# Kernel optimization log

Hardware: AMD Instinct MI355X
Metric: run time of the kernel (lower is better)

Reference implementation:

```python
import jax, jax.numpy as jnp
import numpy as np

B, S, H, D = 2, 2048, 2048, 256  # batch, seq, hidden, head_dim
NH, NKV = 8, 1                   # attention heads, kv heads
N_REP = NH // NKV
SCALING = D ** -0.5
ROPE_THETA = 10000.0
NEG_INF = -1e9


def rotate_half(x):
    x1, x2 = jnp.split(x, 2, axis=-1)
    return jnp.concatenate((-x2, x1), axis=-1)


def setup_inputs() -> dict:
    key = jax.random.key(0)
    ks = jax.random.split(key, 5)
    hidden_states = jax.random.normal(ks[0], (B, S, H), dtype=jnp.float32)
    # RoPE cos/sin per position, Gemma-style: inv_freq tiled over full head_dim
    inv_freq = 1.0 / (ROPE_THETA ** (np.arange(0, D, 2, dtype=np.float32) / D))  # [D/2]
    pos = np.arange(S, dtype=np.float32)
    freqs = np.outer(pos, inv_freq)                      # [S, D/2]
    emb = np.concatenate([freqs, freqs], axis=-1)        # [S, D]
    cos = jnp.broadcast_to(jnp.asarray(np.cos(emb)), (B, S, D))
    sin = jnp.broadcast_to(jnp.asarray(np.sin(emb)), (B, S, D))
    # additive causal mask [B, 1, S, S]
    causal = jnp.triu(jnp.full((S, S), NEG_INF, dtype=jnp.float32), k=1)
    attention_mask = jnp.broadcast_to(causal[None, None], (B, 1, S, S))
    scale = 0.02
    Wq = jax.random.normal(ks[1], (H, NH * D), dtype=jnp.float32) * scale
    Wk = jax.random.normal(ks[2], (H, NKV * D), dtype=jnp.float32) * scale
    Wv = jax.random.normal(ks[3], (H, NKV * D), dtype=jnp.float32) * scale
    Wo = jax.random.normal(ks[4], (NH * D, H), dtype=jnp.float32) * scale
    return {"hidden_states": hidden_states, "cos": cos, "sin": sin,
            "attention_mask": attention_mask, "Wq": Wq, "Wk": Wk, "Wv": Wv, "Wo": Wo}


def reference(hidden_states, cos, sin, attention_mask, Wq, Wk, Wv, Wo):
    # projections: [B,S,H] @ [H, nh*D] -> [B, nh, S, D]
    q = (hidden_states @ Wq).reshape(B, S, NH, D).transpose(0, 2, 1, 3)
    k = (hidden_states @ Wk).reshape(B, S, NKV, D).transpose(0, 2, 1, 3)
    v = (hidden_states @ Wv).reshape(B, S, NKV, D).transpose(0, 2, 1, 3)
    # RoPE (cos/sin broadcast over head dim via unsqueeze at axis 1)
    c = cos[:, None]  # [B,1,S,D]
    s = sin[:, None]
    q = q * c + rotate_half(q) * s
    k = k * c + rotate_half(k) * s
    # repeat_kv: [B, NKV, S, D] -> [B, NH, S, D]
    k = jnp.repeat(k, N_REP, axis=1)
    v = jnp.repeat(v, N_REP, axis=1)
    # eager attention
    attn_weights = jnp.einsum("bhqd,bhkd->bhqk", q, k) * SCALING
    attn_weights = attn_weights + attention_mask[:, :, :, :S]
    attn_weights = jax.nn.softmax(attn_weights.astype(jnp.float32), axis=-1).astype(q.dtype)
    attn_output = jnp.einsum("bhqk,bhkd->bhqd", attn_weights, v)
    attn_output = attn_output.transpose(0, 2, 1, 3).reshape(B, S, NH * D)
    attn_output = attn_output @ Wo
    return attn_output, attn_weights
```

## Files before the change

kernel.cpp:

```cpp
#include <hip/hip_runtime.h>
#include <hip/hip_bf16.h>

#define B_   2
#define S_   2048
#define H_   2048
#define D_   256
#define NH_  8

typedef unsigned short u16;
typedef __bf16 bf16x8 __attribute__((ext_vector_type(8)));
typedef float f32x4 __attribute__((ext_vector_type(4)));
typedef unsigned int uint4v __attribute__((ext_vector_type(4)));
typedef unsigned int uint2v __attribute__((ext_vector_type(2)));

#define AS1 __attribute__((address_space(1)))
#define AS3 __attribute__((address_space(3)))

__device__ __forceinline__ u16 f2bf(float x) {
  union { float f; unsigned u; } v; v.f = x;
  unsigned u = v.u;
  u += 0x7FFFu + ((u >> 16) & 1u);
  return (u16)(u >> 16);
}
__device__ __forceinline__ float bf2f(u16 x) {
  union { unsigned u; float f; } v; v.u = ((unsigned)x) << 16;
  return v.f;
}

__device__ __forceinline__ void gld_lds16(const u16* g, u16* l) {
  __builtin_amdgcn_global_load_lds((const AS1 unsigned int*)g,
                                   (AS3 unsigned int*)l, 16, 0, 0);
}

#define BM 128
#define BN 128
#define BK 32

enum GemmMode { MODE_PROJ = 0, MODE_QK = 1, MODE_PV = 2, MODE_WO = 3 };

template <int MODE>
__global__ __launch_bounds__(256)
void gemm_nt(const u16* __restrict__ A, const u16* __restrict__ Bb,
             void* __restrict__ Cp, float* __restrict__ rows,
             int K, int lda, int ldb, int ldc)
{
  int bn, bm;
  if constexpr (MODE == MODE_QK) {
    int t = blockIdx.x;
    bm = 0;
    while ((bm + 1) * (bm + 2) / 2 <= t) bm++;
    bn = t - bm * (bm + 1) / 2;
  } else if constexpr (MODE == MODE_PV) {
    bn = blockIdx.x;
    bm = (int)gridDim.y - 1 - (int)blockIdx.y;
  } else {
    bn = blockIdx.x;
    bm = blockIdx.y;
  }
  const int bz = blockIdx.z;
  const int m0 = bm * BM, n0 = bn * BN;

  const u16* Ap = A;
  const u16* Bp = Bb;
  float* Cf = (float*)Cp;
  u16*   Cu = (u16*)Cp;

  if constexpr (MODE == MODE_QK) {
    Ap   += (size_t)bz * S_ * D_;
    Bp   += (size_t)(bz >> 3) * S_ * D_;
    Cu   += (size_t)bz * S_ * S_;
    rows += (size_t)bz * S_;
  } else if constexpr (MODE == MODE_PV) {
    Ap   += (size_t)bz * S_ * S_;
    Bp   += (size_t)(bz >> 3) * D_ * S_;
    Cu   += (size_t)(bz >> 3) * S_ * (NH_ * D_) + (size_t)(bz & 7) * D_;
    rows += (size_t)bz * S_;
  }

  int Keff = K;
  if constexpr (MODE == MODE_PV) {
    int lim = (bm + 1) * BM;
    Keff = lim < K ? lim : K;
  }

  __shared__ __align__(16) u16 As[BM * BK];
  __shared__ __align__(16) u16 Bs[BN * BK];

  const int tid  = threadIdx.x;
  const int lane = tid & 63;
  const int quad = lane >> 4;
  const int l16  = lane & 15;
  const int wave = tid >> 6;
  const int wm   = (wave >> 1) << 6;
  const int wn   = (wave & 1) << 6;

  f32x4 acc[4][4] = {};

  for (int kt = 0; kt < Keff; kt += BK) {
    #pragma unroll
    for (int i = 0; i < 2; i++) {
      int c = tid + i * 256;
      gld_lds16(Ap + (size_t)(m0 + (c >> 2)) * lda + kt + (c & 3) * 8, &As[c * 8]);
    }
    #pragma unroll
    for (int i = 0; i < 2; i++) {
      int c = tid + i * 256;
      gld_lds16(Bp + (size_t)(n0 + (c >> 2)) * ldb + kt + (c & 3) * 8, &Bs[c * 8]);
    }
    __syncthreads();

    bf16x8 af[4], bfr[4];
    #pragma unroll
    for (int i = 0; i < 4; i++)
      af[i] = *(const bf16x8*)(&As[(wm + i * 16 + l16) * BK + quad * 8]);
    #pragma unroll
    for (int j = 0; j < 4; j++)
      bfr[j] = *(const bf16x8*)(&Bs[(wn + j * 16 + l16) * BK + quad * 8]);
    #pragma unroll
    for (int i = 0; i < 4; i++)
      #pragma unroll
      for (int j = 0; j < 4; j++)
        acc[i][j] = __builtin_amdgcn_mfma_f32_16x16x32_bf16(af[i], bfr[j], acc[i][j], 0, 0, 0);
    __syncthreads();
  }

  const float SCL2 = 0.0625f * 1.44269504088896340736f;
  if constexpr (MODE == MODE_WO) {
    #pragma unroll
    for (int i = 0; i < 4; i++) {
      #pragma unroll
      for (int r = 0; r < 4; r++) {
        const int m = m0 + wm + i * 16 + quad * 4 + r;
        #pragma unroll
        for (int j = 0; j < 4; j++) {
          int n = n0 + wn + j * 16 + l16;
          Cf[(size_t)m * ldc + n] = acc[i][j][r];
        }
      }
    }
  } else {
    __shared__ __align__(16) u16 Cs[32][136];
    const int band16 = (wave >> 1) * 16;
    #pragma unroll
    for (int i = 0; i < 4; i++) {
      #pragma unroll
      for (int r = 0; r < 4; r++) {
        const int lr = band16 + quad * 4 + r;
        const int m  = m0 + wm + i * 16 + quad * 4 + r;
        if constexpr (MODE == MODE_QK) {
          float rs = 0.f;
          #pragma unroll
          for (int j = 0; j < 4; j++) {
            int n = n0 + wn + j * 16 + l16;
            float e = (n <= m) ? exp2f(acc[i][j][r] * SCL2) : 0.f;
            rs += e;
            Cs[lr][wn + j * 16 + l16] = f2bf(e);
          }
          #pragma unroll
          for (int o = 1; o < 16; o <<= 1) rs += __shfl_xor(rs, o, 64);
          if (l16 == 0) atomicAdd(&rows[m], rs);
        } else if constexpr (MODE == MODE_PV) {
          const float inv = 1.0f / rows[m];
          #pragma unroll
          for (int j = 0; j < 4; j++)
            Cs[lr][wn + j * 16 + l16] = f2bf(acc[i][j][r] * inv);
        } else {
          #pragma unroll
          for (int j = 0; j < 4; j++)
            Cs[lr][wn + j * 16 + l16] = f2bf(acc[i][j][r]);
        }
      }
      __syncthreads();
      #pragma unroll
      for (int ch = tid; ch < 512; ch += 256) {
        const int rr = ch >> 4, cc = ch & 15;
        const int mg = m0 + ((rr >> 4) << 6) + i * 16 + (rr & 15);
        *(uint4v*)(Cu + (size_t)mg * ldc + n0 + cc * 8) =
            *(const uint4v*)(&Cs[rr][cc * 8]);
      }
      __syncthreads();
    }
  }
}

__global__ __launch_bounds__(256)
void convert_bf16_kernel(const float* __restrict__ src, u16* __restrict__ dst, int n4)
{
  #pragma unroll
  for (int it = 0; it < 4; ++it) {
    int i = it * 524288 + blockIdx.x * 256 + threadIdx.x;
    if (i >= n4) return;
    float4 f = ((const float4*)src)[i];
    uint2v p;
    p.x = (unsigned)f2bf(f.x) | ((unsigned)f2bf(f.y) << 16);
    p.y = (unsigned)f2bf(f.z) | ((unsigned)f2bf(f.w) << 16);
    ((uint2v*)dst)[i] = p;
  }
}

__global__ __launch_bounds__(256)
void transpose_convert(const float* __restrict__ src, u16* __restrict__ dst, int K, int N)
{
  __shared__ float t[32][33];
  int n0 = blockIdx.x * 32, k0 = blockIdx.y * 32;
  int c = threadIdx.x & 31, r = threadIdx.x >> 5;
  #pragma unroll
  for (int rr = 0; rr < 32; rr += 8)
    t[r + rr][c] = src[(size_t)(k0 + r + rr) * N + n0 + c];
  __syncthreads();
  #pragma unroll
  for (int rr = 0; rr < 32; rr += 8)
    dst[(size_t)(n0 + r + rr) * K + k0 + c] = f2bf(t[c][r + rr]);
}

__global__ __launch_bounds__(256)
void transpose_v_kernel(const u16* __restrict__ v, u16* __restrict__ vt)
{
  __shared__ u16 t[32][34];
  int b = blockIdx.z;
  int d0 = blockIdx.x * 32, s0 = blockIdx.y * 32;
  int c = threadIdx.x & 31, r = threadIdx.x >> 5;
  #pragma unroll
  for (int rr = 0; rr < 32; rr += 8)
    t[r + rr][c] = v[(size_t)(b * S_ + s0 + r + rr) * 2560 + 2304 + d0 + c];
  __syncthreads();
  #pragma unroll
  for (int rr = 0; rr < 32; rr += 8)
    vt[(size_t)b * D_ * S_ + (size_t)(d0 + r + rr) * S_ + s0 + c] = t[c][r + rr];
}

__global__ __launch_bounds__(256)
void rope_q_kernel(const u16* __restrict__ qraw, const float* __restrict__ cosb,
                   const float* __restrict__ sinb, u16* __restrict__ qout)
{
  const int d    = threadIdx.x & 127;
  const int half = threadIdx.x >> 7;
  #pragma unroll
  for (int it = 0; it < 16; ++it) {
    int idx = blockIdx.x * 32 + it * 2 + half;
    int h = idx & 7, bs = idx >> 3;
    int b = bs >> 11, s = bs & (S_ - 1);
    size_t base = (size_t)bs * 2560 + (size_t)h * D_;
    float q1 = bf2f(qraw[base + d]);
    float q2 = bf2f(qraw[base + 128 + d]);
    float c  = cosb[(size_t)bs * D_ + d];
    float sn = sinb[(size_t)bs * D_ + d];
    size_t ob = (((size_t)b * NH_ + h) * S_ + s) * D_;
    qout[ob + d]       = f2bf(q1 * c - q2 * sn);
    qout[ob + 128 + d] = f2bf(q2 * c + q1 * sn);
  }
}

__global__ __launch_bounds__(256)
void rope_k_kernel(const u16* __restrict__ kraw, const float* __restrict__ cosb,
                   const float* __restrict__ sinb, u16* __restrict__ kout)
{
  const int d    = threadIdx.x & 127;
  const int half = threadIdx.x >> 7;
  #pragma unroll
  for (int it = 0; it < 8; ++it) {
    int bs = blockIdx.x * 16 + it * 2 + half;
    size_t base = (size_t)bs * 2560 + 2048;
    float k1 = bf2f(kraw[base + d]);
    float k2 = bf2f(kraw[base + 128 + d]);
    float c  = cosb[(size_t)bs * D_ + d];
    float sn = sinb[(size_t)bs * D_ + d];
    kout[(size_t)bs * D_ + d]       = f2bf(k1 * c - k2 * sn);
    kout[(size_t)bs * D_ + 128 + d] = f2bf(k2 * c + k1 * sn);
  }
}

__global__ __launch_bounds__(256)
void normalize_p(const u16* __restrict__ E, const float* __restrict__ rows,
                 float* __restrict__ P)
{
  const int k0 = threadIdx.x * 8;
  for (int rr = 0; rr < 16; ++rr) {
    const int r = blockIdx.x * 16 + rr;
    const int q = r & (S_ - 1);
    const u16* e = E + (size_t)r * S_;
    float* p = P + (size_t)r * S_;
    const float inv = 1.0f / rows[r];

    float4 lo = {0.f, 0.f, 0.f, 0.f}, hi = {0.f, 0.f, 0.f, 0.f};
    if (k0 <= q) {
      uint4v u = *(const uint4v*)(e + k0);
      float v[8];
      v[0] = bf2f(u.x & 0xffff); v[1] = bf2f(u.x >> 16);
      v[2] = bf2f(u.y & 0xffff); v[3] = bf2f(u.y >> 16);
      v[4] = bf2f(u.z & 0xffff); v[5] = bf2f(u.z >> 16);
      v[6] = bf2f(u.w & 0xffff); v[7] = bf2f(u.w >> 16);
      lo.x = (k0 + 0 <= q) ? v[0] * inv : 0.f;
      lo.y = (k0 + 1 <= q) ? v[1] * inv : 0.f;
      lo.z = (k0 + 2 <= q) ? v[2] * inv : 0.f;
      lo.w = (k0 + 3 <= q) ? v[3] * inv : 0.f;
      hi.x = (k0 + 4 <= q) ? v[4] * inv : 0.f;
      hi.y = (k0 + 5 <= q) ? v[5] * inv : 0.f;
      hi.z = (k0 + 6 <= q) ? v[6] * inv : 0.f;
      hi.w = (k0 + 7 <= q) ? v[7] * inv : 0.f;
    }
    *(float4*)(p + k0)     = lo;
    *(float4*)(p + k0 + 4) = hi;
  }
}

extern "C" void kernel_launch(void* const* d_in, const int* in_sizes, int n_in,
                              void* d_out, int out_size, void* d_ws, size_t ws_size,
                              hipStream_t stream)
{
  const float* X    = (const float*)d_in[0];
  const float* cosb = (const float*)d_in[1];
  const float* sinb = (const float*)d_in[2];
  const float* Wq   = (const float*)d_in[4];
  const float* Wk   = (const float*)d_in[5];
  const float* Wv   = (const float*)d_in[6];
  const float* Wo   = (const float*)d_in[7];

  float* outO = (float*)d_out;
  float* outP = outO + (size_t)B_ * S_ * H_;

  u16* ws     = (u16*)d_ws;
  u16* Xbf    = ws;
  u16* WT     = Xbf    + 8388608;
  u16* WoT    = WT     + 5242880;
  u16* QKVraw = WoT    + 4194304;
  u16* Qbf    = QKVraw + 10485760;
  u16* Kbf    = Qbf    + 8388608;
  u16* VT     = Kbf    + 1048576;
  u16* AObf   = VT     + 1048576;
  u16* Ebf    = AObf   + 8388608;
  float* Rows = (float*)(Ebf + 67108864);

  convert_bf16_kernel<<<2048, 256, 0, stream>>>(X, Xbf, 2097152);
  transpose_convert<<<dim3(64, 64), 256, 0, stream>>>(Wq, WT, 2048, 2048);
  transpose_convert<<<dim3(8, 64),  256, 0, stream>>>(Wk, WT + 2048 * 2048, 2048, 256);
  transpose_convert<<<dim3(8, 64),  256, 0, stream>>>(Wv, WT + 2304 * 2048, 2048, 256);
  transpose_convert<<<dim3(64, 64), 256, 0, stream>>>(Wo, WoT, 2048, 2048);
  gemm_nt<MODE_PROJ><<<dim3(20, 32, 1), 256, 0, stream>>>(
      Xbf, WT, QKVraw, nullptr, 2048, 2048, 2048, 2560);
  rope_q_kernel<<<1024, 256, 0, stream>>>(QKVraw, cosb, sinb, Qbf);
  rope_k_kernel<<<256, 256, 0, stream>>>(QKVraw, cosb, sinb, Kbf);
  transpose_v_kernel<<<dim3(8, 64, 2), 256, 0, stream>>>(QKVraw, VT);
  hipMemsetAsync(Rows, 0, 32768 * sizeof(float), stream);
  gemm_nt<MODE_QK><<<dim3(136, 1, 16), 256, 0, stream>>>(
      Qbf, Kbf, Ebf, Rows, 256, 256, 256, 2048);
  normalize_p<<<2048, 256, 0, stream>>>(Ebf, Rows, outP);
  gemm_nt<MODE_PV><<<dim3(2, 16, 16), 256, 0, stream>>>(
      Ebf, VT, AObf, Rows, 2048, 2048, 2048, 2048);
  gemm_nt<MODE_WO><<<dim3(16, 32, 1), 256, 0, stream>>>(
      AObf, WoT, outO, nullptr, 2048, 2048, 2048, 2048);
}
```

Before: 694.2 us.

## Fuse P normalization into PV GEMM and merge prep/postproj kernels

```diff
diff --git a/kernel.cpp b/kernel.cpp
--- a/kernel.cpp
+++ b/kernel.cpp
@@ -42,6 +42,7 @@
 __global__ __launch_bounds__(256)
 void gemm_nt(const u16* __restrict__ A, const u16* __restrict__ Bb,
              void* __restrict__ Cp, float* __restrict__ rows,
+             float* __restrict__ Pout,
              int K, int lda, int ldb, int ldc)
 {
   int bn, bm;
@@ -64,6 +65,7 @@
   const u16* Bp = Bb;
   float* Cf = (float*)Cp;
   u16*   Cu = (u16*)Cp;
+  float* Pp = Pout;
 
   if constexpr (MODE == MODE_QK) {
     Ap   += (size_t)bz * S_ * D_;
@@ -75,6 +77,7 @@
     Bp   += (size_t)(bz >> 3) * D_ * S_;
     Cu   += (size_t)(bz >> 3) * S_ * (NH_ * D_) + (size_t)(bz & 7) * D_;
     rows += (size_t)bz * S_;
+    Pp   += (size_t)bz * S_ * S_;
   }
 
   int Keff = K;
@@ -83,8 +86,10 @@
     Keff = lim < K ? lim : K;
   }
 
-  __shared__ __align__(16) u16 As[BM * BK];
-  __shared__ __align__(16) u16 Bs[BN * BK];
+  __shared__ __align__(16) u16 smem[BM * BK + BN * BK + 512];
+  u16* As = smem;
+  u16* Bs = smem + BM * BK;
+  __shared__ float invs[BM];
 
   const int tid  = threadIdx.x;
   const int lane = tid & 63;
@@ -94,6 +99,10 @@
   const int wm   = (wave >> 1) << 6;
   const int wn   = (wave & 1) << 6;
 
+  if constexpr (MODE == MODE_PV) {
+    if (tid < BM) invs[tid] = 1.0f / rows[m0 + tid];
+  }
+
   f32x4 acc[4][4] = {};
 
   for (int kt = 0; kt < Keff; kt += BK) {
@@ -121,25 +130,65 @@
       #pragma unroll
       for (int j = 0; j < 4; j++)
         acc[i][j] = __builtin_amdgcn_mfma_f32_16x16x32_bf16(af[i], bfr[j], acc[i][j], 0, 0, 0);
+
+    if constexpr (MODE == MODE_PV) {
+      if (bn == 0) {
+        const int r8 = tid >> 3;
+        const int c8 = tid & 7;
+        #pragma unroll
+        for (int rr = 0; rr < BM; rr += 32) {
+          const int r = rr + r8;
+          const u16* e = &As[r * BK + c8 * 4];
+          const float inv = invs[r];
+          float4 o;
+          o.x = bf2f(e[0]) * inv; o.y = bf2f(e[1]) * inv;
+          o.z = bf2f(e[2]) * inv; o.w = bf2f(e[3]) * inv;
+          *(float4*)(Pp + (size_t)(m0 + r) * S_ + kt + c8 * 4) = o;
+        }
+      }
+    }
     __syncthreads();
+  }
+
+  if constexpr (MODE == MODE_PV) {
+    if (bn == 0 && Keff < S_) {
+      const int r8 = tid >> 3;
+      const int c8 = tid & 7;
+      const float4 z = {0.f, 0.f, 0.f, 0.f};
+      #pragma unroll
+      for (int rr = 0; rr < BM; rr += 32) {
+        float* pr = Pp + (size_t)(m0 + rr + r8) * S_;
+        for (int c4 = (Keff >> 2) + c8; c4 < (S_ >> 2); c4 += 8)
+          *(float4*)(pr + c4 * 4) = z;
+      }
+    }
   }
 
   const float SCL2 = 0.0625f * 1.44269504088896340736f;
   if constexpr (MODE == MODE_WO) {
+    float (*Cs32)[132] = (float (*)[132])smem;
+    const int band16 = (wave >> 1) * 16;
     #pragma unroll
     for (int i = 0; i < 4; i++) {
       #pragma unroll
       for (int r = 0; r < 4; r++) {
-        const int m = m0 + wm + i * 16 + quad * 4 + r;
+        const int lr = band16 + quad * 4 + r;
         #pragma unroll
-        for (int j = 0; j < 4; j++) {
-          int n = n0 + wn + j * 16 + l16;
-          Cf[(size_t)m * ldc + n] = acc[i][j][r];
-        }
-      }
+        for (int j = 0; j < 4; j++)
+          Cs32[lr][wn + j * 16 + l16] = acc[i][j][r];
+      }
+      __syncthreads();
+      #pragma unroll
+      for (int ch = tid; ch < 1024; ch += 256) {
+        const int rr = ch >> 5, cc = ch & 31;
+        const int mg = m0 + ((rr >> 4) << 6) + i * 16 + (rr & 15);
+        *(float4*)(Cf + (size_t)mg * ldc + n0 + cc * 4) =
+            *(const float4*)(&Cs32[rr][cc * 4]);
+      }
+      __syncthreads();
     }
   } else {
-    __shared__ __align__(16) u16 Cs[32][136];
+    u16 (*Cs)[136] = (u16 (*)[136])smem;
     const int band16 = (wave >> 1) * 16;
     #pragma unroll
     for (int i = 0; i < 4; i++) {
@@ -160,7 +209,7 @@
           for (int o = 1; o < 16; o <<= 1) rs += __shfl_xor(rs, o, 64);
           if (l16 == 0) atomicAdd(&rows[m], rs);
         } else if constexpr (MODE == MODE_PV) {
-          const float inv = 1.0f / rows[m];
+          const float inv = invs[wm + i * 16 + quad * 4 + r];
           #pragma unroll
           for (int j = 0; j < 4; j++)
             Cs[lr][wn + j * 16 + l16] = f2bf(acc[i][j][r] * inv);
@@ -183,26 +232,10 @@
   }
 }
 
-__global__ __launch_bounds__(256)
-void convert_bf16_kernel(const float* __restrict__ src, u16* __restrict__ dst, int n4)
-{
-  #pragma unroll
-  for (int it = 0; it < 4; ++it) {
-    int i = it * 524288 + blockIdx.x * 256 + threadIdx.x;
-    if (i >= n4) return;
-    float4 f = ((const float4*)src)[i];
-    uint2v p;
-    p.x = (unsigned)f2bf(f.x) | ((unsigned)f2bf(f.y) << 16);
-    p.y = (unsigned)f2bf(f.z) | ((unsigned)f2bf(f.w) << 16);
-    ((uint2v*)dst)[i] = p;
-  }
-}
-
-__global__ __launch_bounds__(256)
-void transpose_convert(const float* __restrict__ src, u16* __restrict__ dst, int K, int N)
-{
-  __shared__ float t[32][33];
-  int n0 = blockIdx.x * 32, k0 = blockIdx.y * 32;
+__device__ __forceinline__ void tc_tile(const float* __restrict__ src,
+                                        u16* __restrict__ dst, int K, int N,
+                                        int n0, int k0, float (*t)[33])
+{
   int c = threadIdx.x & 31, r = threadIdx.x >> 5;
   #pragma unroll
   for (int rr = 0; rr < 32; rr += 8)
@@ -214,93 +247,90 @@
 }
 
 __global__ __launch_bounds__(256)
-void transpose_v_kernel(const u16* __restrict__ v, u16* __restrict__ vt)
+void prep_kernel(const float* __restrict__ X,
+                 const float* __restrict__ Wq, const float* __restrict__ Wk,
+                 const float* __restrict__ Wv, const float* __restrict__ Wo,
+                 u16* __restrict__ Xbf, u16* __restrict__ WT,
+                 u16* __restrict__ WoT)
+{
+  __shared__ float t[32][33];
+  const int bid = blockIdx.x;
+  if (bid < 4096) {
+    tc_tile(Wq, WT, 2048, 2048, (bid & 63) * 32, (bid >> 6) * 32, t);
+  } else if (bid < 4608) {
+    int l = bid - 4096;
+    tc_tile(Wk, WT + 2048 * 2048, 2048, 256, (l & 7) * 32, (l >> 3) * 32, t);
+  } else if (bid < 5120) {
+    int l = bid - 4608;
+    tc_tile(Wv, WT + 2304 * 2048, 2048, 256, (l & 7) * 32, (l >> 3) * 32, t);
+  } else if (bid < 9216) {
+    int l = bid - 5120;
+    tc_tile(Wo, WoT, 2048, 2048, (l & 63) * 32, (l >> 6) * 32, t);
+  } else {
+    int l = bid - 9216;
+    #pragma unroll
+    for (int it = 0; it < 4; ++it) {
+      int i = it * 524288 + l * 256 + threadIdx.x;
+      float4 f = ((const float4*)X)[i];
+      uint2v p;
+      p.x = (unsigned)f2bf(f.x) | ((unsigned)f2bf(f.y) << 16);
+      p.y = (unsigned)f2bf(f.z) | ((unsigned)f2bf(f.w) << 16);
+      ((uint2v*)Xbf)[i] = p;
+    }
+  }
+}
+
+__global__ __launch_bounds__(256)
+void postproj_kernel(const u16* __restrict__ raw, const float* __restrict__ cosb,
+                     const float* __restrict__ sinb, u16* __restrict__ qout,
+                     u16* __restrict__ kout, u16* __restrict__ vt)
 {
   __shared__ u16 t[32][34];
-  int b = blockIdx.z;
-  int d0 = blockIdx.x * 32, s0 = blockIdx.y * 32;
-  int c = threadIdx.x & 31, r = threadIdx.x >> 5;
-  #pragma unroll
-  for (int rr = 0; rr < 32; rr += 8)
-    t[r + rr][c] = v[(size_t)(b * S_ + s0 + r + rr) * 2560 + 2304 + d0 + c];
-  __syncthreads();
-  #pragma unroll
-  for (int rr = 0; rr < 32; rr += 8)
-    vt[(size_t)b * D_ * S_ + (size_t)(d0 + r + rr) * S_ + s0 + c] = t[c][r + rr];
-}
-
-__global__ __launch_bounds__(256)
-void rope_q_kernel(const u16* __restrict__ qraw, const float* __restrict__ cosb,
-                   const float* __restrict__ sinb, u16* __restrict__ qout)
-{
-  const int d    = threadIdx.x & 127;
-  const int half = threadIdx.x >> 7;
-  #pragma unroll
-  for (int it = 0; it < 16; ++it) {
-    int idx = blockIdx.x * 32 + it * 2 + half;
-    int h = idx & 7, bs = idx >> 3;
-    int b = bs >> 11, s = bs & (S_ - 1);
-    size_t base = (size_t)bs * 2560 + (size_t)h * D_;
-    float q1 = bf2f(qraw[base + d]);
-    float q2 = bf2f(qraw[base + 128 + d]);
-    float c  = cosb[(size_t)bs * D_ + d];
-    float sn = sinb[(size_t)bs * D_ + d];
-    size_t ob = (((size_t)b * NH_ + h) * S_ + s) * D_;
-    qout[ob + d]       = f2bf(q1 * c - q2 * sn);
-    qout[ob + 128 + d] = f2bf(q2 * c + q1 * sn);
-  }
-}
-
-__global__ __launch_bounds__(256)
-void rope_k_kernel(const u16* __restrict__ kraw, const float* __restrict__ cosb,
-                   const float* __restrict__ sinb, u16* __restrict__ kout)
-{
-  const int d    = threadIdx.x & 127;
-  const int half = threadIdx.x >> 7;
-  #pragma unroll
-  for (int it = 0; it < 8; ++it) {
-    int bs = blockIdx.x * 16 + it * 2 + half;
-    size_t base = (size_t)bs * 2560 + 2048;
-    float k1 = bf2f(kraw[base + d]);
-    float k2 = bf2f(kraw[base + 128 + d]);
-    float c  = cosb[(size_t)bs * D_ + d];
-    float sn = sinb[(size_t)bs * D_ + d];
-    kout[(size_t)bs * D_ + d]       = f2bf(k1 * c - k2 * sn);
-    kout[(size_t)bs * D_ + 128 + d] = f2bf(k2 * c + k1 * sn);
-  }
-}
-
-__global__ __launch_bounds__(256)
-void normalize_p(const u16* __restrict__ E, const float* __restrict__ rows,
-                 float* __restrict__ P)
-{
-  const int k0 = threadIdx.x * 8;
-  for (int rr = 0; rr < 16; ++rr) {
-    const int r = blockIdx.x * 16 + rr;
-    const int q = r & (S_ - 1);
-    const u16* e = E + (size_t)r * S_;
-    float* p = P + (size_t)r * S_;
-    const float inv = 1.0f / rows[r];
-
-    float4 lo = {0.f, 0.f, 0.f, 0.f}, hi = {0.f, 0.f, 0.f, 0.f};
-    if (k0 <= q) {
-      uint4v u = *(const uint4v*)(e + k0);
-      float v[8];
-      v[0] = bf2f(u.x & 0xffff); v[1] = bf2f(u.x >> 16);
-      v[2] = bf2f(u.y & 0xffff); v[3] = bf2f(u.y >> 16);
-      v[4] = bf2f(u.z & 0xffff); v[5] = bf2f(u.z >> 16);
-      v[6] = bf2f(u.w & 0xffff); v[7] = bf2f(u.w >> 16);
-      lo.x = (k0 + 0 <= q) ? v[0] * inv : 0.f;
-      lo.y = (k0 + 1 <= q) ? v[1] * inv : 0.f;
-      lo.z = (k0 + 2 <= q) ? v[2] * inv : 0.f;
-      lo.w = (k0 + 3 <= q) ? v[3] * inv : 0.f;
-      hi.x = (k0 + 4 <= q) ? v[4] * inv : 0.f;
-      hi.y = (k0 + 5 <= q) ? v[5] * inv : 0.f;
-      hi.z = (k0 + 6 <= q) ? v[6] * inv : 0.f;
-      hi.w = (k0 + 7 <= q) ? v[7] * inv : 0.f;
-    }
-    *(float4*)(p + k0)     = lo;
-    *(float4*)(p + k0 + 4) = hi;
+  const int bid = blockIdx.x;
+  if (bid < 1024) {
+    const int d    = threadIdx.x & 127;
+    const int half = threadIdx.x >> 7;
+    #pragma unroll
+    for (int it = 0; it < 16; ++it) {
+      int idx = bid * 32 + it * 2 + half;
+      int h = idx & 7, bs = idx >> 3;
+      int b = bs >> 11, s = bs & (S_ - 1);
+      size_t base = (size_t)bs * 2560 + (size_t)h * D_;
+      float q1 = bf2f(raw[base + d]);
+      float q2 = bf2f(raw[base + 128 + d]);
+      float c  = cosb[(size_t)bs * D_ + d];
+      float sn = sinb[(size_t)bs * D_ + d];
+      size_t ob = (((size_t)b * NH_ + h) * S_ + s) * D_;
+      qout[ob + d]       = f2bf(q1 * c - q2 * sn);
+      qout[ob + 128 + d] = f2bf(q2 * c + q1 * sn);
+    }
+  } else if (bid < 1280) {
+    const int l    = bid - 1024;
+    const int d    = threadIdx.x & 127;
+    const int half = threadIdx.x >> 7;
+    #pragma unroll
+    for (int it = 0; it < 8; ++it) {
+      int bs = l * 16 + it * 2 + half;
+      size_t base = (size_t)bs * 2560 + 2048;
+      float k1 = bf2f(raw[base + d]);
+      float k2 = bf2f(raw[base + 128 + d]);
+      float c  = cosb[(size_t)bs * D_ + d];
+      float sn = sinb[(size_t)bs * D_ + d];
+      kout[(size_t)bs * D_ + d]       = f2bf(k1 * c - k2 * sn);
+      kout[(size_t)bs * D_ + 128 + d] = f2bf(k2 * c + k1 * sn);
+    }
+  } else {
+    int l = bid - 1280;
+    int b = l >> 9, rem = l & 511;
+    int d0 = (rem & 7) * 32, s0 = (rem >> 3) * 32;
+    int c = threadIdx.x & 31, r = threadIdx.x >> 5;
+    #pragma unroll
+    for (int rr = 0; rr < 32; rr += 8)
+      t[r + rr][c] = raw[(size_t)(b * S_ + s0 + r + rr) * 2560 + 2304 + d0 + c];
+    __syncthreads();
+    #pragma unroll
+    for (int rr = 0; rr < 32; rr += 8)
+      vt[(size_t)b * D_ * S_ + (size_t)(d0 + r + rr) * S_ + s0 + c] = t[c][r + rr];
   }
 }
 
@@ -331,22 +361,15 @@
   u16* Ebf    = AObf   + 8388608;
   float* Rows = (float*)(Ebf + 67108864);
 
-  convert_bf16_kernel<<<2048, 256, 0, stream>>>(X, Xbf, 2097152);
-  transpose_convert<<<dim3(64, 64), 256, 0, stream>>>(Wq, WT, 2048, 2048);
-  transpose_convert<<<dim3(8, 64),  256, 0, stream>>>(Wk, WT + 2048 * 2048, 2048, 256);
-  transpose_convert<<<dim3(8, 64),  256, 0, stream>>>(Wv, WT + 2304 * 2048, 2048, 256);
-  transpose_convert<<<dim3(64, 64), 256, 0, stream>>>(Wo, WoT, 2048, 2048);
+  prep_kernel<<<11264, 256, 0, stream>>>(X, Wq, Wk, Wv, Wo, Xbf, WT, WoT);
   gemm_nt<MODE_PROJ><<<dim3(20, 32, 1), 256, 0, stream>>>(
-      Xbf, WT, QKVraw, nullptr, 2048, 2048, 2048, 2560);
-  rope_q_kernel<<<1024, 256, 0, stream>>>(QKVraw, cosb, sinb, Qbf);
-  rope_k_kernel<<<256, 256, 0, stream>>>(QKVraw, cosb, sinb, Kbf);
-  transpose_v_kernel<<<dim3(8, 64, 2), 256, 0, stream>>>(QKVraw, VT);
+      Xbf, WT, QKVraw, nullptr, nullptr, 2048, 2048, 2048, 2560);
+  postproj_kernel<<<2304, 256, 0, stream>>>(QKVraw, cosb, sinb, Qbf, Kbf, VT);
   hipMemsetAsync(Rows, 0, 32768 * sizeof(float), stream);
   gemm_nt<MODE_QK><<<dim3(136, 1, 16), 256, 0, stream>>>(
-      Qbf, Kbf, Ebf, Rows, 256, 256, 256, 2048);
-  normalize_p<<<2048, 256, 0, stream>>>(Ebf, Rows, outP);
+      Qbf, Kbf, Ebf, Rows, nullptr, 256, 256, 256, 2048);
   gemm_nt<MODE_PV><<<dim3(2, 16, 16), 256, 0, stream>>>(
-      Ebf, VT, AObf, Rows, 2048, 2048, 2048, 2048);
+      Ebf, VT, AObf, Rows, outP, 2048, 2048, 2048, 2048);
   gemm_nt<MODE_WO><<<dim3(16, 32, 1), 256, 0, stream>>>(
-      AObf, WoT, outO, nullptr, 2048, 2048, 2048, 2048);
-}
+      AObf, WoT, outO, nullptr, nullptr, 2048, 2048, 2048, 2048);
+}
```

After: 638.5 us. -8.0%, faster.
